# Performance work log

Hardware: AMD Instinct MI355X
Metric: run time of the kernel (lower is better)

Reference implementation:

```python
import jax, jax.numpy as jnp
import numpy as np

B, L, C = 4, 2048, 1024
H = 16
D = C // H  # 64
MAX_SCALE_MUL = float(np.log(100.0))


def setup_inputs() -> dict:
    key = jax.random.key(0)
    ks = jax.random.split(key, 8)
    x = jax.random.normal(ks[0], (B, L, C), dtype=jnp.float32)
    attn_bias = jax.random.normal(ks[1], (1, H, L, L), dtype=jnp.float32) * 0.02
    # nn.Linear(C, 3C, bias=False): weight [3C, C], init ~ U(-1/sqrt(C), 1/sqrt(C))
    lim = 1.0 / np.sqrt(C)
    W_qkv = jax.random.uniform(ks[2], (3 * C, C), minval=-lim, maxval=lim, dtype=jnp.float32)
    q_bias = jnp.zeros((C,), dtype=jnp.float32)
    v_bias = jnp.zeros((C,), dtype=jnp.float32)
    scale_mul_log = jnp.full((1, H, 1, 1), np.log(4.0), dtype=jnp.float32)
    W_proj = jax.random.uniform(ks[3], (C, C), minval=-lim, maxval=lim, dtype=jnp.float32)
    b_proj = jax.random.uniform(ks[4], (C,), minval=-lim, maxval=lim, dtype=jnp.float32)
    return {"x": x, "attn_bias": attn_bias, "W_qkv": W_qkv, "q_bias": q_bias,
            "v_bias": v_bias, "scale_mul_log": scale_mul_log,
            "W_proj": W_proj, "b_proj": b_proj}


def reference(x, attn_bias, W_qkv, q_bias, v_bias, scale_mul_log, W_proj, b_proj):
    Bc, Lc, Cc = x.shape
    qkv_bias = jnp.concatenate([q_bias, jnp.zeros_like(q_bias), v_bias])
    qkv = x @ W_qkv.T + qkv_bias                      # [B, L, 3C]
    qkv = qkv.reshape(Bc, Lc, 3, H, D)
    q, k, v = jnp.moveaxis(qkv, 2, 0)                 # each [B, L, H, D]
    q = jnp.swapaxes(q, 1, 2)                         # [B, H, L, D]
    k = jnp.swapaxes(k, 1, 2)
    v = jnp.swapaxes(v, 1, 2)
    # L2-norm cosine attention with learned per-head scale
    scale_mul = jnp.exp(jnp.minimum(scale_mul_log, MAX_SCALE_MUL))  # [1, H, 1, 1]
    q = q / jnp.linalg.norm(q, axis=-1, keepdims=True).clip(1e-12) * scale_mul
    k = k / jnp.linalg.norm(k, axis=-1, keepdims=True).clip(1e-12)
    attn = jnp.einsum('bhqd,bhkd->bhqk', q, k) + attn_bias
    attn = jax.nn.softmax(attn, axis=-1)
    out = jnp.einsum('bhqk,bhkd->bhqd', attn, v)      # [B, H, L, D]
    out = jnp.swapaxes(out, 1, 2).reshape(Bc, Lc, Cc)
    return out @ W_proj.T + b_proj
```

## Files before the change

### kernel.cpp

```cpp
#include <hip/hip_runtime.h>
#include <cstdint>
#include <cstddef>

#define BATCH 4
#define SEQ   2048
#define CMOD  1024
#define NH    16
#define DH    64
#define LOG100 4.6051701859880914f
#define LOG2E  1.4426950408889634f

typedef __attribute__((ext_vector_type(8))) short bf16x8;
typedef __attribute__((ext_vector_type(4))) float f32x4;
typedef __attribute__((ext_vector_type(16))) float f32x16;

__device__ __forceinline__ float u32lo_f(uint32_t u) {
    union { uint32_t i; float f; } x; x.i = u << 16; return x.f;
}
__device__ __forceinline__ float u32hi_f(uint32_t u) {
    union { uint32_t i; float f; } x; x.i = u & 0xFFFF0000u; return x.f;
}
__device__ __forceinline__ uint16_t f2bf(float f) {
    union { float f; uint32_t i; } x; x.f = f;
    uint32_t u = x.i;
    return (uint16_t)((u + 0x7FFFu + ((u >> 16) & 1u)) >> 16);
}
__device__ __forceinline__ float exp2_fast(float x) {
    float r; asm("v_exp_f32 %0, %1" : "=v"(r) : "v"(x)); return r;
}
__device__ __forceinline__ uint32_t cvt_pk_bf16(float lo, float hi) {
    uint32_t r;
    asm("v_cvt_pk_bf16_f32 %0, %1, %2" : "=v"(r) : "v"(lo), "v"(hi));
    return r;
}
__device__ __forceinline__ void p32swap(uint32_t& x, uint32_t& y) {
#if __has_builtin(__builtin_amdgcn_permlane32_swap)
    auto r = __builtin_amdgcn_permlane32_swap(x, y, false, false);
    x = r[0]; y = r[1];
#else
    asm volatile("v_permlane32_swap_b32 %0, %1\n\ts_nop 1" : "+v"(x), "+v"(y));
#endif
}

__device__ __forceinline__ void gload_lds16(const void* g, void* l) {
    __builtin_amdgcn_global_load_lds(
        (const __attribute__((address_space(1))) uint32_t*)g,
        (__attribute__((address_space(3))) uint32_t*)l,
        16, 0, 0);
}

__global__ __launch_bounds__(256) void cvt_kernel(const float* __restrict__ in,
                                                  uint16_t* __restrict__ out, int n) {
    int i = (blockIdx.x * 256 + threadIdx.x) * 4;
    if (i >= n) return;
    float4 f = *(const float4*)(in + i);
    ushort4 o;
    o.x = f2bf(f.x); o.y = f2bf(f.y); o.z = f2bf(f.z); o.w = f2bf(f.w);
    *(ushort4*)(out + i) = o;
}

__global__ __launch_bounds__(256) void gemm_bt_kernel(
    const uint16_t* __restrict__ A, const uint16_t* __restrict__ B,
    int M, int N, int K, int mode,
    uint16_t* __restrict__ qb, uint16_t* __restrict__ kb, uint16_t* __restrict__ vtb,
    const float* __restrict__ q_bias, const float* __restrict__ v_bias,
    const float* __restrict__ scale_mul_log,
    float* __restrict__ outp, const float* __restrict__ b_proj)
{
    __shared__ __align__(16) uint16_t As[128 * 32];
    __shared__ __align__(16) uint16_t Bs[128 * 32];
    const int t = threadIdx.x;
    const int wave = t >> 6, lane = t & 63;
    const int g = lane >> 4, c16 = lane & 15;
    const int m0 = blockIdx.x * 128, n0 = blockIdx.y * 128;
    const int wm = (wave >> 1) * 64, wn = (wave & 1) * 64;

    f32x4 acc[4][4];
#pragma unroll
    for (int mt = 0; mt < 4; mt++)
#pragma unroll
        for (int nt = 0; nt < 4; nt++) acc[mt][nt] = (f32x4){0.f, 0.f, 0.f, 0.f};

    for (int k0 = 0; k0 < K; k0 += 32) {
        __syncthreads();
#pragma unroll
        for (int i = 0; i < 2; i++) {
            int cc = i * 256 + t;
            int row = cc >> 2, col = (cc & 3) * 8;
            gload_lds16(A + (size_t)(m0 + row) * K + k0 + col, &As[cc * 8]);
            gload_lds16(B + (size_t)(n0 + row) * K + k0 + col, &Bs[cc * 8]);
        }
        __syncthreads();
        bf16x8 af[4], bfv[4];
#pragma unroll
        for (int mt = 0; mt < 4; mt++)
            af[mt] = *(const bf16x8*)&As[(wm + mt * 16 + c16) * 32 + g * 8];
#pragma unroll
        for (int nt = 0; nt < 4; nt++)
            bfv[nt] = *(const bf16x8*)&Bs[(wn + nt * 16 + c16) * 32 + g * 8];
#pragma unroll
        for (int mt = 0; mt < 4; mt++)
#pragma unroll
            for (int nt = 0; nt < 4; nt++)
                acc[mt][nt] = __builtin_amdgcn_mfma_f32_16x16x32_bf16(af[mt], bfv[nt], acc[mt][nt], 0, 0, 0);
    }

    if (mode == 0) {
        const int colbase = n0 + wn;
        const int tt = colbase >> 10;
        const int cc0 = colbase & 1023;
        const int hh = cc0 >> 6;
        float qmul = 1.0f;
        if (tt == 0) qmul = __expf(fminf(scale_mul_log[hh], LOG100)) * LOG2E;
#pragma unroll
        for (int mt = 0; mt < 4; mt++) {
            float vals[4][4];
            float n2[4] = {0.f, 0.f, 0.f, 0.f};
#pragma unroll
            for (int nt = 0; nt < 4; nt++) {
                const int ci = cc0 + nt * 16 + c16;
                float badd = 0.f;
                if (tt == 0) badd = q_bias[ci];
                else if (tt == 2) badd = v_bias[ci];
#pragma unroll
                for (int r = 0; r < 4; r++) {
                    float v = acc[mt][nt][r] + badd;
                    vals[nt][r] = v;
                    n2[r] += v * v;
                }
            }
            float rs[4];
            if (tt < 2) {
#pragma unroll
                for (int r = 0; r < 4; r++) {
                    float s = n2[r];
                    s += __shfl_xor(s, 1, 64);
                    s += __shfl_xor(s, 2, 64);
                    s += __shfl_xor(s, 4, 64);
                    s += __shfl_xor(s, 8, 64);
                    rs[r] = qmul / fmaxf(sqrtf(s), 1e-12f);
                }
            } else {
#pragma unroll
                for (int r = 0; r < 4; r++) rs[r] = 1.0f;
            }
#pragma unroll
            for (int nt = 0; nt < 4; nt++) {
                const int dd = (cc0 + nt * 16 + c16) & 63;
#pragma unroll
                for (int r = 0; r < 4; r++) {
                    const int row = m0 + wm + mt * 16 + g * 4 + r;
                    const int bb = row >> 11, ll = row & 2047;
                    const size_t bhx = (size_t)bb * NH + hh;
                    const uint16_t val = f2bf(vals[nt][r] * rs[r]);
                    if (tt < 2) {
                        size_t addr = ((bhx * 64 + (ll >> 5)) * 4 + (dd >> 4)) * 512
                                      + ((dd >> 3) & 1) * 256 + (ll & 31) * 8 + (dd & 7);
                        if (tt == 0) qb[addr] = val; else kb[addr] = val;
                    } else {
                        size_t addr = ((bhx * 64 + (ll >> 5)) * 4 + (dd >> 5) * 2 + ((ll >> 4) & 1)) * 512
                                      + (((ll >> 3) & 1) * 32 + (dd & 31)) * 8 + (ll & 7);
                        vtb[addr] = val;
                    }
                }
            }
        }
    } else {
#pragma unroll
        for (int mt = 0; mt < 4; mt++)
#pragma unroll
            for (int nt = 0; nt < 4; nt++)
#pragma unroll
                for (int r = 0; r < 4; r++) {
                    int row = m0 + wm + mt * 16 + g * 4 + r;
                    int col = n0 + wn + nt * 16 + c16;
                    outp[(size_t)row * N + col] = acc[mt][nt][r] + b_proj[col];
                }
    }
}

__global__ __launch_bounds__(512, 4) void attn_kernel(
    const uint16_t* __restrict__ qfrag, const uint16_t* __restrict__ kfrag,
    const uint16_t* __restrict__ vfrag, const float* __restrict__ bias,
    uint16_t* __restrict__ ob)
{
    __shared__ __align__(16) uint16_t KsL[2 * 4 * 4 * 512];
    __shared__ __align__(16) uint2    Bsh[2 * 512];

    const int t = threadIdx.x;
    const int w8 = t >> 6, lane = t & 63;
    const int b = w8 & 3, qhalf = w8 >> 2;
    const int c32 = lane & 31, hi = lane >> 5;

    const int bid = blockIdx.x;
    const int xcd = bid & 7;
    const int inner = bid >> 3;
    const int h = xcd * 2 + (inner & 1);
    const int qt = inner >> 1;
    const int q0w = qt * 64 + qhalf * 32;
    const size_t bh = (size_t)b * NH + h;

    bf16x8 qf[4];
#pragma unroll
    for (int s = 0; s < 4; s++)
        qf[s] = *(const bf16x8*)(qfrag +
            ((bh * 64 + (size_t)(qt * 2 + qhalf)) * 4 + s) * 512 + hi * 256 + c32 * 8);

    auto stage = [&](int tl, int buf) {
#pragma unroll
        for (int j = 0; j < 2; j++) {
            int u = w8 * 2 + j;
            int bb = u >> 2, s = u & 3;
            gload_lds16(kfrag + (((size_t)bb * NH + h) * 64 + tl) * 4 * 512 + s * 512 + lane * 8,
                        &KsL[((buf * 4 + bb) * 4 + s) * 512 + lane * 8]);
        }
    };

    const uint16_t* vbase = vfrag + ((bh * 64) * 4) * 512 + lane * 8;

    const int brow = t >> 3, kch = t & 7;
    const float* bgl = bias + ((size_t)h * SEQ + qt * 64 + brow) * SEQ + kch * 4;
    const int u0 = (kch >> 1) * 128 + (brow >> 5) * 64 + (kch & 1) * 32 + (brow & 31);

    auto writeBsh = [&](int buf, float4 a) {
        Bsh[buf * 512 + u0] =
            make_uint2(cvt_pk_bf16(a.x * LOG2E, a.y * LOG2E),
                       cvt_pk_bf16(a.z * LOG2E, a.w * LOG2E));
    };

    f32x16 accO[2];
#pragma unroll
    for (int db = 0; db < 2; db++)
#pragma unroll
        for (int i = 0; i < 16; i++) accO[db][i] = 0.f;
    float lrun = 0.f;

    float4 a0 = *(const float4*)(bgl);
    float4 br0 = *(const float4*)(bgl + 32);
    stage(0, 0);
    writeBsh(0, a0);
    __syncthreads();

    for (int it = 0; it < 64; ++it) {
        const int cur = it & 1;

        bf16x8 vf[4];
#pragma unroll
        for (int j = 0; j < 4; j++)
            vf[j] = *(const bf16x8*)(vbase + ((size_t)it * 4 + j) * 512);

        if (it < 63) {
            const int nb = cur ^ 1;
            writeBsh(nb, br0);
            int n2 = it + 2; if (n2 > 63) n2 = 63;
            br0 = *(const float4*)(bgl + n2 * 32);
            stage(it + 1, nb);
        }

        bf16x8 kf[4];
#pragma unroll
        for (int s = 0; s < 4; s++)
            kf[s] = *(const bf16x8*)&KsL[((cur * 4 + b) * 4 + s) * 512 + lane * 8];

        f32x16 S;
#pragma unroll
        for (int i = 0; i < 16; i++) S[i] = 0.f;
        __builtin_amdgcn_s_setprio(1);
#pragma unroll
        for (int s = 0; s < 4; s++)
            S = __builtin_amdgcn_mfma_f32_32x32x16_bf16(kf[s], qf[s], S, 0, 0, 0);
        __builtin_amdgcn_s_setprio(0);

        float p[16];
        float lp = 0.f;
#pragma unroll
        for (int tt = 0; tt < 4; tt++) {
            uint2 uu = Bsh[cur * 512 + tt * 128 + qhalf * 64 + hi * 32 + c32];
            p[tt * 4 + 0] = exp2_fast(S[tt * 4 + 0] + u32lo_f(uu.x));
            p[tt * 4 + 1] = exp2_fast(S[tt * 4 + 1] + u32hi_f(uu.x));
            p[tt * 4 + 2] = exp2_fast(S[tt * 4 + 2] + u32lo_f(uu.y));
            p[tt * 4 + 3] = exp2_fast(S[tt * 4 + 3] + u32hi_f(uu.y));
            lp += (p[tt * 4 + 0] + p[tt * 4 + 1]) + (p[tt * 4 + 2] + p[tt * 4 + 3]);
        }
        lrun += lp;

        bf16x8 pa[2];
#pragma unroll
        for (int cp = 0; cp < 2; cp++) {
            uint32_t X0 = cvt_pk_bf16(p[8 * cp + 0], p[8 * cp + 1]);
            uint32_t X1 = cvt_pk_bf16(p[8 * cp + 2], p[8 * cp + 3]);
            uint32_t Y0 = cvt_pk_bf16(p[8 * cp + 4], p[8 * cp + 5]);
            uint32_t Y1 = cvt_pk_bf16(p[8 * cp + 6], p[8 * cp + 7]);
            p32swap(X0, Y0);
            p32swap(X1, Y1);
            union { uint32_t u[4]; bf16x8 v; } pu;
            pu.u[0] = X0; pu.u[1] = X1; pu.u[2] = Y0; pu.u[3] = Y1;
            pa[cp] = pu.v;
        }

        __builtin_amdgcn_s_setprio(1);
#pragma unroll
        for (int c = 0; c < 2; c++)
#pragma unroll
            for (int db = 0; db < 2; db++)
                accO[db] = __builtin_amdgcn_mfma_f32_32x32x16_bf16(pa[c], vf[db * 2 + c], accO[db], 0, 0, 0);
        __builtin_amdgcn_s_setprio(0);

        __syncthreads();
    }

    float s = lrun + __shfl_xor(lrun, 32, 64);
    float inv = 1.0f / s;
    float linv[16];
#pragma unroll
    for (int r = 0; r < 16; r++)
        linv[r] = __shfl(inv, (r & 3) + 8 * (r >> 2) + 4 * hi, 64);
#pragma unroll
    for (int r = 0; r < 16; r++) {
        int rowq = (r & 3) + 8 * (r >> 2) + 4 * hi;
        size_t rowbase = ((size_t)b * SEQ + q0w + rowq) * CMOD + h * DH;
        ob[rowbase + c32]      = f2bf(accO[0][r] * linv[r]);
        ob[rowbase + 32 + c32] = f2bf(accO[1][r] * linv[r]);
    }
}

extern "C" void kernel_launch(void* const* d_in, const int* in_sizes, int n_in,
                              void* d_out, int out_size, void* d_ws, size_t ws_size,
                              hipStream_t stream) {
    const float* x             = (const float*)d_in[0];
    const float* attn_bias     = (const float*)d_in[1];
    const float* W_qkv         = (const float*)d_in[2];
    const float* q_bias        = (const float*)d_in[3];
    const float* v_bias        = (const float*)d_in[4];
    const float* scale_mul_log = (const float*)d_in[5];
    const float* W_proj        = (const float*)d_in[6];
    const float* b_proj        = (const float*)d_in[7];
    float* out = (float*)d_out;

    uint8_t* ws = (uint8_t*)d_ws;
    size_t off = 0;
    auto alloc = [&](size_t bytes) { uint8_t* p = ws + off; off += (bytes + 255) & ~(size_t)255; return p; };
    uint16_t* xb     = (uint16_t*)alloc((size_t)8192 * 1024 * 2);
    uint16_t* wqkvb  = (uint16_t*)alloc((size_t)3072 * 1024 * 2);
    uint16_t* wprojb = (uint16_t*)alloc((size_t)1024 * 1024 * 2);
    uint16_t* qb     = (uint16_t*)alloc((size_t)BATCH * NH * SEQ * DH * 2);
    uint16_t* kb     = (uint16_t*)alloc((size_t)BATCH * NH * SEQ * DH * 2);
    uint16_t* vtb    = (uint16_t*)alloc((size_t)BATCH * NH * SEQ * DH * 2);
    uint16_t* ob     = (uint16_t*)alloc((size_t)BATCH * SEQ * CMOD * 2);
    (void)ws_size;

    cvt_kernel<<<8192, 256, 0, stream>>>(x, xb, 8388608);
    cvt_kernel<<<3072, 256, 0, stream>>>(W_qkv, wqkvb, 3145728);
    cvt_kernel<<<1024, 256, 0, stream>>>(W_proj, wprojb, 1048576);

    dim3 g1(64, 24);
    gemm_bt_kernel<<<g1, 256, 0, stream>>>(xb, wqkvb, 8192, 3072, 1024, 0,
                                           qb, kb, vtb, q_bias, v_bias, scale_mul_log,
                                           nullptr, nullptr);

    attn_kernel<<<512, 512, 0, stream>>>(qb, kb, vtb, attn_bias, ob);

    dim3 g3(64, 8);
    gemm_bt_kernel<<<g3, 256, 0, stream>>>(ob, wprojb, 8192, 1024, 1024, 1,
                                           nullptr, nullptr, nullptr, nullptr, nullptr, nullptr,
                                           out, b_proj);
}
```

Baseline: 288.6 us.

## Process two key tiles per iteration to halve barriers and deepen prefetch

The attention main loop now handles two 32-key tiles per iteration, giving 32 iterations instead of 64. K staging and bias buffers are doubled so each stage covers both tiles, which halves the number of __syncthreads barriers. The loads of the second V tile are issued after the first QK MFMA chain so their latency is hidden. This raises LDS use (KsL doubles to 64KB) and register pressure, which may lower occupancy under launch_bounds(512,4).

```diff
diff --git a/kernel.cpp b/kernel.cpp
--- a/kernel.cpp
+++ b/kernel.cpp
@@ -184,8 +184,8 @@
     const uint16_t* __restrict__ vfrag, const float* __restrict__ bias,
     uint16_t* __restrict__ ob)
 {
-    __shared__ __align__(16) uint16_t KsL[2 * 4 * 4 * 512];
-    __shared__ __align__(16) uint2    Bsh[2 * 512];
+    __shared__ __align__(16) uint16_t KsL[2 * 4 * 8 * 512];
+    __shared__ __align__(16) uint2    Bsh[2 * 2 * 512];
 
     const int t = threadIdx.x;
     const int w8 = t >> 6, lane = t & 63;
@@ -206,26 +206,33 @@
         qf[s] = *(const bf16x8*)(qfrag +
             ((bh * 64 + (size_t)(qt * 2 + qhalf)) * 4 + s) * 512 + hi * 256 + c32 * 8);
 
-    auto stage = [&](int tl, int buf) {
-#pragma unroll
-        for (int j = 0; j < 2; j++) {
-            int u = w8 * 2 + j;
-            int bb = u >> 2, s = u & 3;
+    auto stage = [&](int it2, int buf) {
+#pragma unroll
+        for (int j = 0; j < 4; j++) {
+            int u = w8 * 4 + j;
+            int bb = u >> 3, sl = u & 7;
+            int tl = 2 * it2 + (sl >> 2), s = sl & 3;
             gload_lds16(kfrag + (((size_t)bb * NH + h) * 64 + tl) * 4 * 512 + s * 512 + lane * 8,
-                        &KsL[((buf * 4 + bb) * 4 + s) * 512 + lane * 8]);
+                        &KsL[((buf * 4 + bb) * 8 + sl) * 512 + lane * 8]);
         }
     };
 
     const uint16_t* vbase = vfrag + ((bh * 64) * 4) * 512 + lane * 8;
 
     const int brow = t >> 3, kch = t & 7;
-    const float* bgl = bias + ((size_t)h * SEQ + qt * 64 + brow) * SEQ + kch * 4;
-    const int u0 = (kch >> 1) * 128 + (brow >> 5) * 64 + (kch & 1) * 32 + (brow & 31);
-
-    auto writeBsh = [&](int buf, float4 a) {
-        Bsh[buf * 512 + u0] =
-            make_uint2(cvt_pk_bf16(a.x * LOG2E, a.y * LOG2E),
-                       cvt_pk_bf16(a.z * LOG2E, a.w * LOG2E));
+    const float* bgl = bias + ((size_t)h * SEQ + qt * 64 + brow) * SEQ + kch * 8;
+
+    auto writeBsh = [&](int buf, float4 a, float4 b4) {
+#pragma unroll
+        for (int e = 0; e < 2; e++) {
+            int g = kch * 2 + e;
+            int kb2 = g >> 3, gg = g & 7;
+            int unit = (gg >> 1) * 128 + (brow >> 5) * 64 + (gg & 1) * 32 + (brow & 31);
+            float4 v = e ? b4 : a;
+            Bsh[(buf * 2 + kb2) * 512 + unit] =
+                make_uint2(cvt_pk_bf16(v.x * LOG2E, v.y * LOG2E),
+                           cvt_pk_bf16(v.z * LOG2E, v.w * LOG2E));
+        }
     };
 
     f32x16 accO[2];
@@ -236,75 +243,93 @@
     float lrun = 0.f;
 
     float4 a0 = *(const float4*)(bgl);
-    float4 br0 = *(const float4*)(bgl + 32);
+    float4 a1 = *(const float4*)(bgl + 4);
+    float4 br0 = *(const float4*)(bgl + 64);
+    float4 br1 = *(const float4*)(bgl + 68);
     stage(0, 0);
-    writeBsh(0, a0);
+    writeBsh(0, a0, a1);
     __syncthreads();
 
-    for (int it = 0; it < 64; ++it) {
+    for (int it = 0; it < 32; ++it) {
         const int cur = it & 1;
 
-        bf16x8 vf[4];
-#pragma unroll
-        for (int j = 0; j < 4; j++)
-            vf[j] = *(const bf16x8*)(vbase + ((size_t)it * 4 + j) * 512);
-
-        if (it < 63) {
+        bf16x8 vf0[4];
+        {
+            const uint16_t* vp = vbase + ((size_t)(2 * it) * 4) * 512;
+#pragma unroll
+            for (int j = 0; j < 4; j++) vf0[j] = *(const bf16x8*)(vp + j * 512);
+        }
+
+        if (it < 31) {
             const int nb = cur ^ 1;
-            writeBsh(nb, br0);
-            int n2 = it + 2; if (n2 > 63) n2 = 63;
-            br0 = *(const float4*)(bgl + n2 * 32);
+            writeBsh(nb, br0, br1);
+            int n2 = it + 2; if (n2 > 31) n2 = 31;
+            br0 = *(const float4*)(bgl + (size_t)n2 * 64);
+            br1 = *(const float4*)(bgl + (size_t)n2 * 64 + 4);
             stage(it + 1, nb);
         }
 
-        bf16x8 kf[4];
-#pragma unroll
-        for (int s = 0; s < 4; s++)
-            kf[s] = *(const bf16x8*)&KsL[((cur * 4 + b) * 4 + s) * 512 + lane * 8];
-
-        f32x16 S;
-#pragma unroll
-        for (int i = 0; i < 16; i++) S[i] = 0.f;
-        __builtin_amdgcn_s_setprio(1);
-#pragma unroll
-        for (int s = 0; s < 4; s++)
-            S = __builtin_amdgcn_mfma_f32_32x32x16_bf16(kf[s], qf[s], S, 0, 0, 0);
-        __builtin_amdgcn_s_setprio(0);
-
-        float p[16];
-        float lp = 0.f;
-#pragma unroll
-        for (int tt = 0; tt < 4; tt++) {
-            uint2 uu = Bsh[cur * 512 + tt * 128 + qhalf * 64 + hi * 32 + c32];
-            p[tt * 4 + 0] = exp2_fast(S[tt * 4 + 0] + u32lo_f(uu.x));
-            p[tt * 4 + 1] = exp2_fast(S[tt * 4 + 1] + u32hi_f(uu.x));
-            p[tt * 4 + 2] = exp2_fast(S[tt * 4 + 2] + u32lo_f(uu.y));
-            p[tt * 4 + 3] = exp2_fast(S[tt * 4 + 3] + u32hi_f(uu.y));
-            lp += (p[tt * 4 + 0] + p[tt * 4 + 1]) + (p[tt * 4 + 2] + p[tt * 4 + 3]);
-        }
-        lrun += lp;
-
+        bf16x8 vf1[4];
         bf16x8 pa[2];
-#pragma unroll
-        for (int cp = 0; cp < 2; cp++) {
-            uint32_t X0 = cvt_pk_bf16(p[8 * cp + 0], p[8 * cp + 1]);
-            uint32_t X1 = cvt_pk_bf16(p[8 * cp + 2], p[8 * cp + 3]);
-            uint32_t Y0 = cvt_pk_bf16(p[8 * cp + 4], p[8 * cp + 5]);
-            uint32_t Y1 = cvt_pk_bf16(p[8 * cp + 6], p[8 * cp + 7]);
-            p32swap(X0, Y0);
-            p32swap(X1, Y1);
-            union { uint32_t u[4]; bf16x8 v; } pu;
-            pu.u[0] = X0; pu.u[1] = X1; pu.u[2] = Y0; pu.u[3] = Y1;
-            pa[cp] = pu.v;
-        }
-
-        __builtin_amdgcn_s_setprio(1);
-#pragma unroll
-        for (int c = 0; c < 2; c++)
-#pragma unroll
-            for (int db = 0; db < 2; db++)
-                accO[db] = __builtin_amdgcn_mfma_f32_32x32x16_bf16(pa[c], vf[db * 2 + c], accO[db], 0, 0, 0);
-        __builtin_amdgcn_s_setprio(0);
+
+#pragma unroll
+        for (int kb2 = 0; kb2 < 2; kb2++) {
+            bf16x8 kf[4];
+#pragma unroll
+            for (int s = 0; s < 4; s++)
+                kf[s] = *(const bf16x8*)&KsL[((cur * 4 + b) * 8 + kb2 * 4 + s) * 512 + lane * 8];
+
+            f32x16 S;
+#pragma unroll
+            for (int i = 0; i < 16; i++) S[i] = 0.f;
+            __builtin_amdgcn_s_setprio(1);
+#pragma unroll
+            for (int s = 0; s < 4; s++)
+                S = __builtin_amdgcn_mfma_f32_32x32x16_bf16(kf[s], qf[s], S, 0, 0, 0);
+            __builtin_amdgcn_s_setprio(0);
+
+            if (kb2 == 0) {
+                const uint16_t* vp = vbase + ((size_t)(2 * it + 1) * 4) * 512;
+#pragma unroll
+                for (int j = 0; j < 4; j++) vf1[j] = *(const bf16x8*)(vp + j * 512);
+            }
+
+            float p[16];
+            float lp = 0.f;
+#pragma unroll
+            for (int tt = 0; tt < 4; tt++) {
+                uint2 uu = Bsh[(cur * 2 + kb2) * 512 + tt * 128 + qhalf * 64 + hi * 32 + c32];
+                p[tt * 4 + 0] = exp2_fast(S[tt * 4 + 0] + u32lo_f(uu.x));
+                p[tt * 4 + 1] = exp2_fast(S[tt * 4 + 1] + u32hi_f(uu.x));
+                p[tt * 4 + 2] = exp2_fast(S[tt * 4 + 2] + u32lo_f(uu.y));
+                p[tt * 4 + 3] = exp2_fast(S[tt * 4 + 3] + u32hi_f(uu.y));
+                lp += (p[tt * 4 + 0] + p[tt * 4 + 1]) + (p[tt * 4 + 2] + p[tt * 4 + 3]);
+            }
+            lrun += lp;
+
+#pragma unroll
+            for (int cp = 0; cp < 2; cp++) {
+                uint32_t X0 = cvt_pk_bf16(p[8 * cp + 0], p[8 * cp + 1]);
+                uint32_t X1 = cvt_pk_bf16(p[8 * cp + 2], p[8 * cp + 3]);
+                uint32_t Y0 = cvt_pk_bf16(p[8 * cp + 4], p[8 * cp + 5]);
+                uint32_t Y1 = cvt_pk_bf16(p[8 * cp + 6], p[8 * cp + 7]);
+                p32swap(X0, Y0);
+                p32swap(X1, Y1);
+                union { uint32_t u[4]; bf16x8 v; } pu;
+                pu.u[0] = X0; pu.u[1] = X1; pu.u[2] = Y0; pu.u[3] = Y1;
+                pa[cp] = pu.v;
+            }
+
+            __builtin_amdgcn_s_setprio(1);
+#pragma unroll
+            for (int c = 0; c < 2; c++)
+#pragma unroll
+                for (int db = 0; db < 2; db++) {
+                    bf16x8 vv = kb2 ? vf1[db * 2 + c] : vf0[db * 2 + c];
+                    accO[db] = __builtin_amdgcn_mfma_f32_32x32x16_bf16(pa[c], vv, accO[db], 0, 0, 0);
+                }
+            __builtin_amdgcn_s_setprio(0);
+        }
 
         __syncthreads();
     }
```

New measurement: 315.9 us. 1.09x slower.
